# Performance work log

Measured on AMD Instinct MI355X. Metric: run time of the kernel, lower is better.

The kernel has to match this reference:

```python
import jax, jax.numpy as jnp
import numpy as np

HID, QLORA, NH = 5120, 1536, 128
NOPE, ROPE, KVLORA = 128, 64, 512
QHD = NOPE + ROPE  # 192
VHD = 128
SCALE = QHD ** (-0.5) * 0.707
EPS = 1e-6


def rmsnorm(x, w):
    xf = x.astype(jnp.float32)
    var = jnp.mean(xf * xf, axis=-1, keepdims=True)
    return (w * (xf * jax.lax.rsqrt(var + EPS))).astype(x.dtype)


def setup_inputs() -> dict:
    key = jax.random.key(0)
    ks = jax.random.split(key, 10)
    b, q, past = 2, 512, 512
    s = 0.02
    return {
        "hidden_states": jax.random.normal(ks[0], (b, q, HID), jnp.float32),
        "attention_mask": jnp.zeros((b, 1, q, past + q), jnp.float32),
        "past_key": jax.random.normal(ks[1], (b, NH, past, QHD), jnp.float32),
        "past_value": jax.random.normal(ks[2], (b, NH, past, VHD), jnp.float32),
        "w_q_a": jax.random.normal(ks[3], (QLORA, HID), jnp.float32) * s,
        "g_q_a": jnp.ones((QLORA,), jnp.float32),
        "w_q_b": jax.random.normal(ks[4], (NH * QHD, QLORA), jnp.float32) * s,
        "w_kv_a": jax.random.normal(ks[5], (KVLORA + ROPE, HID), jnp.float32) * s,
        "g_kv_a": jnp.ones((KVLORA,), jnp.float32),
        "w_kv_b": jax.random.normal(ks[6], (NH * (NOPE + VHD), KVLORA), jnp.float32) * s,
    }


def reference(hidden_states, attention_mask, past_key, past_value,
              w_q_a, g_q_a, w_q_b, w_kv_a, g_kv_a, w_kv_b):
    b, q_len, _ = hidden_states.shape
    # Q path: low-rank down-proj -> RMSNorm -> up-proj
    q = rmsnorm(hidden_states @ w_q_a.T, g_q_a) @ w_q_b.T
    q = q.reshape(b, q_len, NH, QHD).transpose(0, 2, 1, 3)  # [b,h,q,192]
    q_nope, q_pe = q[..., :NOPE], q[..., NOPE:]
    # KV path: joint down-proj, split latent / rope key
    ckv = hidden_states @ w_kv_a.T                          # [b,q,576]
    compressed_kv, k_pe = ckv[..., :KVLORA], ckv[..., KVLORA:]
    kv = rmsnorm(compressed_kv, g_kv_a) @ w_kv_b.T
    kv = kv.reshape(b, q_len, NH, NOPE + VHD).transpose(0, 2, 1, 3)
    k_nope, value_states = kv[..., :NOPE], kv[..., NOPE:]
    k_pe = k_pe.reshape(b, 1, q_len, ROPE)                  # shared across heads
    query_states = jnp.concatenate([q_nope, q_pe], axis=-1)
    key_states = jnp.concatenate(
        [k_nope, jnp.broadcast_to(k_pe, (b, NH, q_len, ROPE))], axis=-1)
    key_states = jnp.concatenate([past_key, key_states], axis=2)
    value_states = jnp.concatenate([past_value, value_states], axis=2)
    scores = jnp.einsum('bhqd,bhkd->bhqk', query_states, key_states) * SCALE
    scores = scores + attention_mask
    attn = jax.nn.softmax(scores.astype(jnp.float32), axis=-1).astype(query_states.dtype)
    attn_output = jnp.einsum('bhqk,bhkv->bhqv', attn, value_states)
    return attn_output, key_states, value_states
```

## Files before the change

### kernel.cpp

```cpp
#include <hip/hip_runtime.h>

#define NB    2
#define QLEN  512
#define HIDD  5120
#define QLORA 1536
#define NHEAD 128
#define QHD   192
#define VHD   128
#define KVTOT 1024

typedef float          f32x4   __attribute__((ext_vector_type(4)));
typedef __bf16         bf16x8  __attribute__((ext_vector_type(8)));
typedef unsigned short u16x8   __attribute__((ext_vector_type(8)));
typedef unsigned short u16x4   __attribute__((ext_vector_type(4)));

static __device__ __forceinline__ unsigned short f2bf(float f) {
  union { float f; unsigned u; } v; v.f = f;
  return (unsigned short)((v.u + 0x7fffu + ((v.u >> 16) & 1u)) >> 16);
}

static __device__ __forceinline__ void g2l16(const void* g, void* l) {
  __builtin_amdgcn_global_load_lds(
      (const __attribute__((address_space(1))) void*)g,
      (__attribute__((address_space(3))) void*)l, 16, 0, 0);
}

__global__ __launch_bounds__(256) void zero_pad_k(unsigned short* __restrict__ dst) {
  int i = blockIdx.x * 256 + threadIdx.x;
  u16x8 z = {0, 0, 0, 0, 0, 0, 0, 0};
  *(u16x8*)(dst + (long)i * 8) = z;
}

struct CvtArgs {
  const float* src[5];
  unsigned short* dst[5];
  int off[6];
};

__global__ __launch_bounds__(256) void cvt_all_k(CvtArgs a) {
  int b = blockIdx.x, s = 0;
  #pragma unroll
  for (int k = 0; k < 4; ++k) if (b >= a.off[k + 1]) s = k + 1;
  long lb = b - a.off[s];
  const float* in = a.src[s];
  unsigned short* out = a.dst[s];
  long base = lb * 1024 + threadIdx.x;
  #pragma unroll
  for (int k = 0; k < 4; ++k) {
    long i = base + k * 256;
    f32x4 v = *(const f32x4*)(in + i * 4);
    u16x4 o;
    o[0] = f2bf(v[0]); o[1] = f2bf(v[1]); o[2] = f2bf(v[2]); o[3] = f2bf(v[3]);
    *(u16x4*)(out + i * 4) = o;
  }
}

__global__ __launch_bounds__(256) void flags_k(const float* __restrict__ mask,
                                               int* __restrict__ flags) {
  int id = blockIdx.x;
  int b = id >> 6, qt = (id >> 4) & 3, kt = id & 15;
  const float* base = mask + (long)b * 524288 + (long)qt * 128 * 1024 + kt * 64;
  int t = threadIdx.x, w = t >> 6;
  unsigned acc = 0;
  #pragma unroll
  for (int i = 0; i < 32; ++i) {
    int e = i * 256 + t;
    int r = e >> 6, c = e & 63;
    union { float f; unsigned u; } v; v.f = base[(long)r * 1024 + c];
    acc |= v.u;
  }
  int any = __any(acc != 0);
  __shared__ int sf[4];
  if ((t & 63) == 0) sf[w] = any;
  __syncthreads();
  if (t == 0) flags[id] = sf[0] | sf[1] | sf[2] | sf[3];
}

__global__ __launch_bounds__(256, 4) void gemm_qa_ckv(const unsigned short* __restrict__ A,
                                                      const unsigned short* __restrict__ Bm,
                                                      float* __restrict__ part) {
  __shared__ __align__(16) unsigned short sA[128 * 64];
  __shared__ __align__(16) unsigned short sB[64 * 64];
  const int t = threadIdx.x, w = t >> 6, l = t & 63;
  const int l15 = l & 15, lh = l >> 4;
  const int swz7 = l15 & 7;
  const int id = blockIdx.x;
  const int xcd = id & 7, slot = id >> 3;
  const int pz = xcd + 8 * (slot >> 3);
  const int mb = slot & 7;
  const int z = pz / 34;
  const int nb = pz - z * 34;
  const unsigned short* Ab = A + (long)mb * 128 * HIDD;
  const unsigned short* Bb = Bm + (long)nb * 64 * HIDD;
  f32x4 acc[2][4];
  #pragma unroll
  for (int i = 0; i < 2; ++i)
    #pragma unroll
    for (int j = 0; j < 4; ++j)
      #pragma unroll
      for (int r = 0; r < 4; ++r) acc[i][j][r] = 0.f;

  const int k0 = z * 1280;
  for (int kt = k0; kt < k0 + 1280; kt += 64) {
    #pragma unroll
    for (int i2 = 0; i2 < 4; ++i2) {
      int n = i2 * 256 + t, r = n >> 3, c = (n & 7) ^ (r & 7);
      g2l16(Ab + (long)r * HIDD + kt + c * 8, (char*)sA + (i2 * 256 + w * 64) * 16);
    }
    #pragma unroll
    for (int i2 = 0; i2 < 2; ++i2) {
      int n = i2 * 256 + t, r = n >> 3, c = (n & 7) ^ (r & 7);
      g2l16(Bb + (long)r * HIDD + kt + c * 8, (char*)sB + (i2 * 256 + w * 64) * 16);
    }
    __syncthreads();
    #pragma unroll
    for (int ks = 0; ks < 2; ++ks) {
      bf16x8 af[2], bfr[4];
      #pragma unroll
      for (int i = 0; i < 2; ++i)
        af[i] = *(const bf16x8*)(sA + (w * 32 + i * 16 + l15) * 64 + ((ks * 4 + lh) ^ swz7) * 8);
      #pragma unroll
      for (int j = 0; j < 4; ++j)
        bfr[j] = *(const bf16x8*)(sB + (j * 16 + l15) * 64 + ((ks * 4 + lh) ^ swz7) * 8);
      #pragma unroll
      for (int i = 0; i < 2; ++i)
        #pragma unroll
        for (int j = 0; j < 4; ++j)
          acc[i][j] = __builtin_amdgcn_mfma_f32_16x16x32_bf16(af[i], bfr[j], acc[i][j], 0, 0, 0);
    }
    __syncthreads();
  }
  float* po = part + (long)z * 1024 * 2176;
  const int colbase = nb * 64;
  #pragma unroll
  for (int i = 0; i < 2; ++i)
    #pragma unroll
    for (int j = 0; j < 4; ++j) {
      const int col = colbase + j * 16 + l15;
      #pragma unroll
      for (int r4 = 0; r4 < 4; ++r4) {
        const long row = (long)mb * 128 + w * 32 + i * 16 + lh * 4 + r4;
        po[row * 2176 + col] = acc[i][j][r4];
      }
    }
}

__global__ __launch_bounds__(256) void post_a_k(const float* __restrict__ part,
                                                const float* __restrict__ gq,
                                                const float* __restrict__ gkv,
                                                unsigned short* __restrict__ qan,
                                                unsigned short* __restrict__ ckvn,
                                                float* __restrict__ kout,
                                                unsigned short* __restrict__ kb) {
  const long ZS = 1024L * 2176;
  int bid = blockIdx.x, t = threadIdx.x;
  if (bid >= 2048) {
    int row = bid - 2048;
    int j = t & 63, h0 = t >> 6;
    const float* p = part + (long)row * 2176 + 2048 + j;
    float v = p[0] + p[ZS] + p[2 * ZS] + p[3 * ZS];
    unsigned short vb = f2bf(v);
    long b_ = row >> 9, qi = row & 511;
    for (int h = h0; h < NHEAD; h += 4) {
      long idx = ((b_ * NHEAD + h) * KVTOT + 512 + qi) * QHD + 128 + j;
      kout[idx] = v;
      kb[idx] = vb;
    }
    return;
  }
  bool isQ = bid < 1024;
  int row = isQ ? bid : bid - 1024;
  int cols = isQ ? 1536 : 512;
  const float* g = isQ ? gq : gkv;
  unsigned short* out = isQ ? (qan + (long)row * 1536) : (ckvn + (long)row * 512);
  const float* x = part + (long)row * 2176 + (isQ ? 0 : 1536);
  int w = t >> 6, l = t & 63;
  float xv[6];
  int nc = cols >> 8;
  float ss = 0.f;
  for (int i = 0; i < nc; ++i) {
    int c = t + i * 256;
    float v = x[c] + x[c + ZS] + x[c + 2 * ZS] + x[c + 3 * ZS];
    xv[i] = v; ss += v * v;
  }
  #pragma unroll
  for (int m = 32; m >= 1; m >>= 1) ss += __shfl_xor(ss, m);
  __shared__ float red[4];
  if (l == 0) red[w] = ss;
  __syncthreads();
  float tot = red[0] + red[1] + red[2] + red[3];
  float rs = rsqrtf(tot / (float)cols + 1e-6f);
  for (int i = 0; i < nc; ++i) {
    int c = t + i * 256;
    out[c] = f2bf(g[c] * xv[i] * rs);
  }
}

__global__ __launch_bounds__(256, 4) void gemm_bt2(const unsigned short* __restrict__ Aq,
                                                   const unsigned short* __restrict__ Bq,
                                                   const unsigned short* __restrict__ Akv,
                                                   const unsigned short* __restrict__ Bkv,
                                                   unsigned short* __restrict__ qout,
                                                   float* __restrict__ kout,
                                                   float* __restrict__ vout,
                                                   unsigned short* __restrict__ kb,
                                                   unsigned short* __restrict__ vt) {
  __shared__ __align__(16) unsigned short sA[128 * 64];
  __shared__ __align__(16) unsigned short sB[128 * 64];
  const int t = threadIdx.x, w = t >> 6, l = t & 63;
  const int l15 = l & 15, lh = l >> 4;
  const int swz7 = l15 & 7;
  const int wm = w >> 1, wn = w & 1;
  const int id = blockIdx.x;
  const int xcd = id & 7, slot = id >> 3;
  const int y = xcd + 8 * (slot >> 3);
  const int mb = slot & 7;
  const bool isQ = y < 192;
  const int nb = isQ ? y : y - 192;
  const int K = isQ ? QLORA : 512;
  const unsigned short* Ab = (isQ ? Aq : Akv) + (long)mb * 128 * K;
  const unsigned short* Bb = (isQ ? Bq : Bkv) + (long)nb * 128 * K;
  f32x4 acc[4][4];
  #pragma unroll
  for (int i = 0; i < 4; ++i)
    #pragma unroll
    for (int j = 0; j < 4; ++j)
      #pragma unroll
      for (int r = 0; r < 4; ++r) acc[i][j][r] = 0.f;

  const int srow = l >> 3;
  const int scol = ((l & 7) ^ srow) * 8;

  for (int kt = 0; kt < K; kt += 64) {
    #pragma unroll
    for (int i = 0; i < 4; ++i) {
      const int chunk = i * 4 + w;
      const int r = chunk * 8 + srow;
      g2l16(Ab + (long)r * K + kt + scol, (char*)sA + chunk * 1024);
      g2l16(Bb + (long)r * K + kt + scol, (char*)sB + chunk * 1024);
    }
    __syncthreads();
    #pragma unroll
    for (int ks = 0; ks < 2; ++ks) {
      bf16x8 af[4], bfr[4];
      #pragma unroll
      for (int i = 0; i < 4; ++i)
        af[i] = *(const bf16x8*)(sA + (wm * 64 + i * 16 + l15) * 64 + ((ks * 4 + lh) ^ swz7) * 8);
      #pragma unroll
      for (int j = 0; j < 4; ++j)
        bfr[j] = *(const bf16x8*)(sB + (wn * 64 + j * 16 + l15) * 64 + ((ks * 4 + lh) ^ swz7) * 8);
      #pragma unroll
      for (int i = 0; i < 4; ++i)
        #pragma unroll
        for (int j = 0; j < 4; ++j)
          acc[i][j] = __builtin_amdgcn_mfma_f32_16x16x32_bf16(af[i], bfr[j], acc[i][j], 0, 0, 0);
    }
    __syncthreads();
  }

  const long rowbase = (long)mb * 128 + wm * 64;
  const long b_ = rowbase >> 9;
  const int colbase = nb * 128 + wn * 64;
  #pragma unroll
  for (int i = 0; i < 4; ++i) {
    const long qi0 = (rowbase + i * 16 + lh * 4) & 511;
    #pragma unroll
    for (int j = 0; j < 4; ++j) {
      const int col = colbase + j * 16 + l15;
      if (isQ) {
        const int h = col / QHD, d = col - h * QHD;
        unsigned short* qp = qout + ((b_ * NHEAD + h) * QLEN + qi0) * QHD + d;
        #pragma unroll
        for (int r4 = 0; r4 < 4; ++r4) qp[(long)r4 * QHD] = f2bf(acc[i][j][r4]);
      } else {
        const int h = col >> 8, d = col & 255;
        if (d < 128) {
          const long idx = ((b_ * NHEAD + h) * KVTOT + 512 + qi0) * QHD + d;
          #pragma unroll
          for (int r4 = 0; r4 < 4; ++r4) {
            kout[idx + (long)r4 * QHD] = acc[i][j][r4];
            kb[idx + (long)r4 * QHD] = f2bf(acc[i][j][r4]);
          }
        } else {
          const int dv = d - 128;
          float* vp = vout + ((b_ * NHEAD + h) * KVTOT + 512 + qi0) * VHD + dv;
          u16x4 tv;
          #pragma unroll
          for (int r4 = 0; r4 < 4; ++r4) {
            vp[(long)r4 * VHD] = acc[i][j][r4];
            tv[r4] = f2bf(acc[i][j][r4]);
          }
          *(u16x4*)(vt + ((b_ * NHEAD + h) * VHD + dv) * KVTOT + 512 + qi0) = tv;
        }
      }
    }
  }
}

__global__ __launch_bounds__(256) void copy_key_past_k(const float* __restrict__ pk,
                                                       float* __restrict__ kout,
                                                       unsigned short* __restrict__ kb) {
  long i4 = (long)blockIdx.x * 256 + threadIdx.x;
  f32x4 v = *(const f32x4*)(pk + i4 * 4);
  long e = i4 * 4;
  long bh = e / 98304;
  long rem = e - bh * 98304;
  long oidx = bh * 196608 + rem;
  *(f32x4*)(kout + oidx) = v;
  u16x4 b;
  b[0] = f2bf(v[0]); b[1] = f2bf(v[1]); b[2] = f2bf(v[2]); b[3] = f2bf(v[3]);
  *(u16x4*)(kb + oidx) = b;
}

__global__ __launch_bounds__(256) void vfix_k(const float* __restrict__ pv,
                                              float* __restrict__ outv,
                                              unsigned short* __restrict__ vt) {
  __shared__ __align__(16) unsigned short sT[128 * 72];
  int bh = blockIdx.x >> 3, kt = blockIdx.x & 7;
  int t = threadIdx.x;
  const float* src = pv + ((long)bh * 512 + kt * 64) * VHD;
  float* dstv = outv + ((long)bh * KVTOT + kt * 64) * VHD;
  #pragma unroll
  for (int i = 0; i < 8; ++i) {
    int id = t + i * 256;
    int r = id >> 5, c4 = (id & 31) * 4;
    f32x4 v = *(const f32x4*)(src + (long)r * VHD + c4);
    *(f32x4*)(dstv + (long)r * VHD + c4) = v;
    #pragma unroll
    for (int jj = 0; jj < 4; ++jj) sT[(c4 + jj) * 72 + r] = f2bf(v[jj]);
  }
  __syncthreads();
  #pragma unroll
  for (int i = 0; i < 4; ++i) {
    int id = t + i * 256;
    int d = id >> 3, c = id & 7;
    u16x8 v = *(const u16x8*)(sT + d * 72 + c * 8);
    *(u16x8*)(vt + ((long)bh * VHD + d) * KVTOT + kt * 64 + c * 8) = v;
  }
}

static __device__ __forceinline__ void stage_k_tile(const unsigned short* __restrict__ src,
                                                    char* dstbase, int t) {
  const int w = t >> 6;
  #pragma unroll
  for (int i2 = 0; i2 < 6; ++i2) {
    int n = i2 * 256 + t;
    int r = n / 24, cp = n - r * 24;
    int c = cp ^ (r & 7);
    g2l16(src + (long)r * QHD + c * 8, dstbase + (i2 * 256 + w * 64) * 16);
  }
}

static __device__ __forceinline__ void stage_v_tile(const unsigned short* __restrict__ src,
                                                    char* dstbase, int t) {
  const int w = t >> 6;
  #pragma unroll
  for (int i2 = 0; i2 < 4; ++i2) {
    int n = i2 * 256 + t;
    int r = n >> 3, cp = n & 7;
    int c = cp ^ (r & 7);
    g2l16(src + (long)r * KVTOT + c * 8, dstbase + (i2 * 256 + w * 64) * 16);
  }
}

__global__ __launch_bounds__(256, 2) void attn_k(const unsigned short* __restrict__ Qw,
                                                 const unsigned short* __restrict__ Kb,
                                                 const unsigned short* __restrict__ Vt,
                                                 const float* __restrict__ mask,
                                                 const int* __restrict__ flags,
                                                 float* __restrict__ outp) {
  __shared__ __align__(16) unsigned short sK[2][64 * 192];
  __shared__ __align__(16) unsigned short sV[128 * 64];
  const int t = threadIdx.x, w = t >> 6, l = t & 63;
  const int l15 = l & 15, lh = l >> 4;
  const int raw = blockIdx.x;
  const int xcd = raw & 7, slot = raw >> 3;
  const int bh = xcd * 32 + (slot >> 2), qt = slot & 3;
  const long b_ = bh >> 7;
  const float SCALE = 0.051023330039633184f;
  const int swz = l15 & 7;

  bf16x8 qf[2][6];
  const unsigned short* Qb = Qw + ((long)bh * QLEN + qt * 128 + w * 32) * QHD;
  #pragma unroll
  for (int i = 0; i < 2; ++i)
    #pragma unroll
    for (int ks = 0; ks < 6; ++ks)
      qf[i][ks] = *(const bf16x8*)(Qb + (i * 16 + l15) * QHD + ks * 32 + lh * 8);

  f32x4 o[2][8];
  #pragma unroll
  for (int i = 0; i < 2; ++i)
    #pragma unroll
    for (int j = 0; j < 8; ++j)
      #pragma unroll
      for (int r = 0; r < 4; ++r) o[i][j][r] = 0.f;
  float m_[2][4], l_[2][4];
  #pragma unroll
  for (int i = 0; i < 2; ++i)
    #pragma unroll
    for (int r = 0; r < 4; ++r) { m_[i][r] = -1e30f; l_[i][r] = 0.f; }

  const int qrow0 = qt * 128 + w * 32;
  const unsigned short* Kbh = Kb + (long)bh * KVTOT * QHD;
  const unsigned short* Vbh = Vt + (long)bh * VHD * KVTOT;
  const float* mrow = mask + b_ * 524288 + (long)(qrow0 + lh * 4) * 1024 + l15;
  const int fbase = (int)b_ * 64 + qt * 16;

  stage_k_tile(Kbh, (char*)sK[0], t);
  __syncthreads();

  for (int kt = 0; kt < 16; ++kt) {
    const int cur = kt & 1;
    stage_v_tile(Vbh + kt * 64, (char*)sV, t);
    if (kt < 15) stage_k_tile(Kbh + (long)(kt + 1) * 64 * QHD, (char*)sK[cur ^ 1], t);
    const int flag = flags[fbase + kt];

    const unsigned short* sKc = sK[cur];
    f32x4 s[2][4];
    #pragma unroll
    for (int i = 0; i < 2; ++i)
      #pragma unroll
      for (int j = 0; j < 4; ++j)
        #pragma unroll
        for (int r = 0; r < 4; ++r) s[i][j][r] = 0.f;
    __builtin_amdgcn_s_setprio(1);
    #pragma unroll
    for (int j = 0; j < 4; ++j) {
      #pragma unroll
      for (int ks = 0; ks < 6; ++ks) {
        bf16x8 kf = *(const bf16x8*)(sKc + ((j * 16 + l15) * 24 + ((ks * 4 + lh) ^ swz)) * 8);
        s[0][j] = __builtin_amdgcn_mfma_f32_16x16x32_bf16(qf[0][ks], kf, s[0][j], 0, 0, 0);
        s[1][j] = __builtin_amdgcn_mfma_f32_16x16x32_bf16(qf[1][ks], kf, s[1][j], 0, 0, 0);
      }
    }
    __builtin_amdgcn_s_setprio(0);

    unsigned short pk16[2][4][4];
    #pragma unroll
    for (int i = 0; i < 2; ++i) {
      #pragma unroll
      for (int rg = 0; rg < 4; ++rg) {
        float sc[4];
        if (flag) {
          #pragma unroll
          for (int j = 0; j < 4; ++j)
            sc[j] = s[i][j][rg] * SCALE + mrow[(long)(i * 16 + rg) * 1024 + kt * 64 + j * 16];
        } else {
          #pragma unroll
          for (int j = 0; j < 4; ++j) sc[j] = s[i][j][rg] * SCALE;
        }
        float mx = fmaxf(fmaxf(sc[0], sc[1]), fmaxf(sc[2], sc[3]));
        mx = fmaxf(mx, __shfl_xor(mx, 1));
        mx = fmaxf(mx, __shfl_xor(mx, 2));
        mx = fmaxf(mx, __shfl_xor(mx, 4));
        mx = fmaxf(mx, __shfl_xor(mx, 8));
        float mo = m_[i][rg];
        float mn = fmaxf(mo, mx);
        if (__any(mn > mo)) {
          float al = __expf(mo - mn);
          #pragma unroll
          for (int jj = 0; jj < 8; ++jj) o[i][jj][rg] *= al;
          l_[i][rg] *= al;
          m_[i][rg] = mn;
        }
        float ps = 0.f;
        #pragma unroll
        for (int j = 0; j < 4; ++j) {
          float p = __expf(sc[j] - m_[i][rg]);
          ps += p;
          pk16[i][rg][j] = f2bf(p);
        }
        l_[i][rg] += ps;
      }
    }
    __syncthreads();

    unsigned short* sPc = (unsigned short*)sK[cur];
    #pragma unroll
    for (int i = 0; i < 2; ++i)
      #pragma unroll
      for (int rg = 0; rg < 4; ++rg) {
        const int prow = w * 32 + i * 16 + lh * 4 + rg;
        #pragma unroll
        for (int j = 0; j < 4; ++j)
          sPc[prow * 72 + j * 16 + l15] = pk16[i][rg][j];
      }

    __builtin_amdgcn_s_setprio(1);
    #pragma unroll
    for (int ks = 0; ks < 2; ++ks) {
      bf16x8 pf0 = *(const bf16x8*)(sPc + (w * 32 + l15) * 72 + ks * 32 + lh * 8);
      bf16x8 pf1 = *(const bf16x8*)(sPc + (w * 32 + 16 + l15) * 72 + ks * 32 + lh * 8);
      #pragma unroll
      for (int jj = 0; jj < 8; ++jj) {
        bf16x8 vf = *(const bf16x8*)(sV + ((jj * 16 + l15) * 8 + ((ks * 4 + lh) ^ swz)) * 8);
        o[0][jj] = __builtin_amdgcn_mfma_f32_16x16x32_bf16(pf0, vf, o[0][jj], 0, 0, 0);
        o[1][jj] = __builtin_amdgcn_mfma_f32_16x16x32_bf16(pf1, vf, o[1][jj], 0, 0, 0);
      }
    }
    __builtin_amdgcn_s_setprio(0);
    __syncthreads();
  }

  #pragma unroll
  for (int i = 0; i < 2; ++i) {
    #pragma unroll
    for (int rg = 0; rg < 4; ++rg) {
      float ls = l_[i][rg];
      ls += __shfl_xor(ls, 1);
      ls += __shfl_xor(ls, 2);
      ls += __shfl_xor(ls, 4);
      ls += __shfl_xor(ls, 8);
      float inv = 1.0f / ls;
      long row = (long)bh * QLEN + qrow0 + i * 16 + lh * 4 + rg;
      #pragma unroll
      for (int jj = 0; jj < 8; ++jj)
        outp[row * VHD + jj * 16 + l15] = o[i][jj][rg] * inv;
    }
  }
}

#define WS_HID_BF   0L
#define WS_WQA_BF   10485760L
#define WS_WQB_BF   32768000L
#define WS_WKVB_BF  108265472L
#define WS_QAN_BF   141819904L
#define WS_CKVN_BF  144965632L
#define WS_Q_BF     146014208L
#define WS_KB_BF    196345856L
#define WS_VT_BF    297009152L
#define WS_FLAGS    364118016L

extern "C" void kernel_launch(void* const* d_in, const int* in_sizes, int n_in,
                              void* d_out, int out_size, void* d_ws, size_t ws_size,
                              hipStream_t stream) {
  const float* hs   = (const float*)d_in[0];
  const float* mask = (const float*)d_in[1];
  const float* pk   = (const float*)d_in[2];
  const float* pv   = (const float*)d_in[3];
  const float* wqa  = (const float*)d_in[4];
  const float* gqa  = (const float*)d_in[5];
  const float* wqb  = (const float*)d_in[6];
  const float* wkva = (const float*)d_in[7];
  const float* gkva = (const float*)d_in[8];
  const float* wkvb = (const float*)d_in[9];

  char* ws = (char*)d_ws;
  unsigned short* hid_bf  = (unsigned short*)(ws + WS_HID_BF);
  unsigned short* wqa_bf  = (unsigned short*)(ws + WS_WQA_BF);
  unsigned short* wkva_bf = wqa_bf + (long)1536 * 5120;
  unsigned short* wpad_bf = wqa_bf + (long)2112 * 5120;
  unsigned short* wqb_bf  = (unsigned short*)(ws + WS_WQB_BF);
  unsigned short* wkvb_bf = (unsigned short*)(ws + WS_WKVB_BF);
  unsigned short* qan_bf  = (unsigned short*)(ws + WS_QAN_BF);
  unsigned short* ckvn_bf = (unsigned short*)(ws + WS_CKVN_BF);
  unsigned short* q_bf    = (unsigned short*)(ws + WS_Q_BF);
  float*          part    = (float*)(ws + WS_Q_BF);
  unsigned short* kb_bf   = (unsigned short*)(ws + WS_KB_BF);
  unsigned short* vt_bf   = (unsigned short*)(ws + WS_VT_BF);
  int*            flags   = (int*)(ws + WS_FLAGS);

  float* out_attn = (float*)d_out;
  float* out_key  = (float*)d_out + 16777216;
  float* out_val  = (float*)d_out + 67108864;

  flags_k<<<128, 256, 0, stream>>>(mask, flags);
  zero_pad_k<<<160, 256, 0, stream>>>(wpad_bf);
  CvtArgs ca;
  ca.src[0] = hs;     ca.dst[0] = hid_bf;
  ca.src[1] = wqa;    ca.dst[1] = wqa_bf;
  ca.src[2] = wkva;   ca.dst[2] = wkva_bf;
  ca.src[3] = wqb;    ca.dst[3] = wqb_bf;
  ca.src[4] = wkvb;   ca.dst[4] = wkvb_bf;
  ca.off[0] = 0; ca.off[1] = 1280; ca.off[2] = 3200; ca.off[3] = 3920;
  ca.off[4] = 13136; ca.off[5] = 17232;
  cvt_all_k<<<17232, 256, 0, stream>>>(ca);
  copy_key_past_k<<<24576, 256, 0, stream>>>(pk, out_key, kb_bf);
  gemm_qa_ckv<<<1088, 256, 0, stream>>>(hid_bf, wqa_bf, part);
  post_a_k<<<3072, 256, 0, stream>>>(part, gqa, gkva, qan_bf, ckvn_bf, out_key, kb_bf);
  gemm_bt2<<<3584, 256, 0, stream>>>(qan_bf, wqb_bf, ckvn_bf, wkvb_bf,
                                     q_bf, out_key, out_val, kb_bf, vt_bf);
  vfix_k<<<2048, 256, 0, stream>>>(pv, out_val, vt_bf);
  attn_k<<<1024, 256, 0, stream>>>(q_bf, kb_bf, vt_bf, mask, flags, out_attn);
}
```

Baseline: 577.6 us.

## Halve split-K in first projection GEMM and load attention V directly into registers

The first down-projection GEMM now splits K into 2 chunks instead of 4, with a smaller grid, so post_a_k only reduces two partial sums. In the attention kernel, V tiles are read straight from global memory into registers instead of being staged through LDS. P gets its own padded LDS buffer, which allows the trailing per-iteration barrier to be removed. This trades fewer partial-sum bytes and fewer LDS round-trips and barriers for less parallelism in the GEMM, and for global V loads that may have higher latency and sit in more registers.

```diff
diff --git a/kernel.cpp b/kernel.cpp
--- a/kernel.cpp
+++ b/kernel.cpp
@@ -88,7 +88,8 @@
   const int xcd = id & 7, slot = id >> 3;
   const int pz = xcd + 8 * (slot >> 3);
   const int mb = slot & 7;
-  const int z = pz / 34;
+  if (pz >= 68) return;
+  const int z = (pz >= 34) ? 1 : 0;
   const int nb = pz - z * 34;
   const unsigned short* Ab = A + (long)mb * 128 * HIDD;
   const unsigned short* Bb = Bm + (long)nb * 64 * HIDD;
@@ -100,8 +101,8 @@
       #pragma unroll
       for (int r = 0; r < 4; ++r) acc[i][j][r] = 0.f;
 
-  const int k0 = z * 1280;
-  for (int kt = k0; kt < k0 + 1280; kt += 64) {
+  const int k0 = z * 2560;
+  for (int kt = k0; kt < k0 + 2560; kt += 64) {
     #pragma unroll
     for (int i2 = 0; i2 < 4; ++i2) {
       int n = i2 * 256 + t, r = n >> 3, c = (n & 7) ^ (r & 7);
@@ -158,7 +159,7 @@
     int row = bid - 2048;
     int j = t & 63, h0 = t >> 6;
     const float* p = part + (long)row * 2176 + 2048 + j;
-    float v = p[0] + p[ZS] + p[2 * ZS] + p[3 * ZS];
+    float v = p[0] + p[ZS];
     unsigned short vb = f2bf(v);
     long b_ = row >> 9, qi = row & 511;
     for (int h = h0; h < NHEAD; h += 4) {
@@ -180,7 +181,7 @@
   float ss = 0.f;
   for (int i = 0; i < nc; ++i) {
     int c = t + i * 256;
-    float v = x[c] + x[c + ZS] + x[c + 2 * ZS] + x[c + 3 * ZS];
+    float v = x[c] + x[c + ZS];
     xv[i] = v; ss += v * v;
   }
   #pragma unroll
@@ -351,18 +352,6 @@
   }
 }
 
-static __device__ __forceinline__ void stage_v_tile(const unsigned short* __restrict__ src,
-                                                    char* dstbase, int t) {
-  const int w = t >> 6;
-  #pragma unroll
-  for (int i2 = 0; i2 < 4; ++i2) {
-    int n = i2 * 256 + t;
-    int r = n >> 3, cp = n & 7;
-    int c = cp ^ (r & 7);
-    g2l16(src + (long)r * KVTOT + c * 8, dstbase + (i2 * 256 + w * 64) * 16);
-  }
-}
-
 __global__ __launch_bounds__(256, 2) void attn_k(const unsigned short* __restrict__ Qw,
                                                  const unsigned short* __restrict__ Kb,
                                                  const unsigned short* __restrict__ Vt,
@@ -370,7 +359,7 @@
                                                  const int* __restrict__ flags,
                                                  float* __restrict__ outp) {
   __shared__ __align__(16) unsigned short sK[2][64 * 192];
-  __shared__ __align__(16) unsigned short sV[128 * 64];
+  __shared__ __align__(16) unsigned short sP[128 * 68];
   const int t = threadIdx.x, w = t >> 6, l = t & 63;
   const int l15 = l & 15, lh = l >> 4;
   const int raw = blockIdx.x;
@@ -403,7 +392,7 @@
 
   const int qrow0 = qt * 128 + w * 32;
   const unsigned short* Kbh = Kb + (long)bh * KVTOT * QHD;
-  const unsigned short* Vbh = Vt + (long)bh * VHD * KVTOT;
+  const unsigned short* Vl = Vt + ((long)bh * VHD + l15) * KVTOT + lh * 8;
   const float* mrow = mask + b_ * 524288 + (long)(qrow0 + lh * 4) * 1024 + l15;
   const int fbase = (int)b_ * 64 + qt * 16;
 
@@ -412,7 +401,12 @@
 
   for (int kt = 0; kt < 16; ++kt) {
     const int cur = kt & 1;
-    stage_v_tile(Vbh + kt * 64, (char*)sV, t);
+    bf16x8 vreg[2][8];
+    #pragma unroll
+    for (int ks = 0; ks < 2; ++ks)
+      #pragma unroll
+      for (int jj = 0; jj < 8; ++jj)
+        vreg[ks][jj] = *(const bf16x8*)(Vl + (long)jj * 16 * KVTOT + kt * 64 + ks * 32);
     if (kt < 15) stage_k_tile(Kbh + (long)(kt + 1) * 64 * QHD, (char*)sK[cur ^ 1], t);
     const int flag = flags[fbase + kt];
 
@@ -474,9 +468,9 @@
         l_[i][rg] += ps;
       }
     }
+
     __syncthreads();
 
-    unsigned short* sPc = (unsigned short*)sK[cur];
     #pragma unroll
     for (int i = 0; i < 2; ++i)
       #pragma unroll
@@ -484,23 +478,21 @@
         const int prow = w * 32 + i * 16 + lh * 4 + rg;
         #pragma unroll
         for (int j = 0; j < 4; ++j)
-          sPc[prow * 72 + j * 16 + l15] = pk16[i][rg][j];
+          sP[prow * 68 + j * 16 + l15] = pk16[i][rg][j];
       }
 
     __builtin_amdgcn_s_setprio(1);
     #pragma unroll
     for (int ks = 0; ks < 2; ++ks) {
-      bf16x8 pf0 = *(const bf16x8*)(sPc + (w * 32 + l15) * 72 + ks * 32 + lh * 8);
-      bf16x8 pf1 = *(const bf16x8*)(sPc + (w * 32 + 16 + l15) * 72 + ks * 32 + lh * 8);
+      bf16x8 pf0 = *(const bf16x8*)(sP + (w * 32 + l15) * 68 + ks * 32 + lh * 8);
+      bf16x8 pf1 = *(const bf16x8*)(sP + (w * 32 + 16 + l15) * 68 + ks * 32 + lh * 8);
       #pragma unroll
       for (int jj = 0; jj < 8; ++jj) {
-        bf16x8 vf = *(const bf16x8*)(sV + ((jj * 16 + l15) * 8 + ((ks * 4 + lh) ^ swz)) * 8);
-        o[0][jj] = __builtin_amdgcn_mfma_f32_16x16x32_bf16(pf0, vf, o[0][jj], 0, 0, 0);
-        o[1][jj] = __builtin_amdgcn_mfma_f32_16x16x32_bf16(pf1, vf, o[1][jj], 0, 0, 0);
+        o[0][jj] = __builtin_amdgcn_mfma_f32_16x16x32_bf16(pf0, vreg[ks][jj], o[0][jj], 0, 0, 0);
+        o[1][jj] = __builtin_amdgcn_mfma_f32_16x16x32_bf16(pf1, vreg[ks][jj], o[1][jj], 0, 0, 0);
       }
     }
     __builtin_amdgcn_s_setprio(0);
-    __syncthreads();
   }
 
   #pragma unroll
@@ -577,7 +569,7 @@
   ca.off[4] = 13136; ca.off[5] = 17232;
   cvt_all_k<<<17232, 256, 0, stream>>>(ca);
   copy_key_past_k<<<24576, 256, 0, stream>>>(pk, out_key, kb_bf);
-  gemm_qa_ckv<<<1088, 256, 0, stream>>>(hid_bf, wqa_bf, part);
+  gemm_qa_ckv<<<576, 256, 0, stream>>>(hid_bf, wqa_bf, part);
   post_a_k<<<3072, 256, 0, stream>>>(part, gqa, gkva, qan_bf, ckvn_bf, out_key, kb_bf);
   gemm_bt2<<<3584, 256, 0, stream>>>(qan_bf, wqb_bf, ckvn_bf, wkvb_bf,
                                      q_bf, out_key, out_val, kb_bf, vt_bf);
```

After: 778.9 us. 1.35x slower.
